# Kernel tuning notes

Hardware: AMD Instinct MI355X
Metric: run time of the kernel (lower is better)

The kernel has to match this reference:

```python
import jax, jax.numpy as jnp
import numpy as np

DIM = 256
NUM_HEADS = 4
HEAD_DIM = DIM // NUM_HEADS
SCALE = HEAD_DIM ** -0.5


def setup_inputs() -> dict:
    key = jax.random.key(0)
    ks = jax.random.split(key, 11)
    B, Nq, Nkv = 4, 2048, 2048
    inp = {
        "query_feat": jax.random.normal(ks[0], (B, Nq, DIM), dtype=jnp.float32),
        "key_value_feat": jax.random.normal(ks[1], (B, Nkv, DIM), dtype=jnp.float32),
        "reliability_kv": jax.random.uniform(ks[2], (B, Nkv), dtype=jnp.float32),
        "Wq": jax.random.normal(ks[3], (DIM, DIM), dtype=jnp.float32) * (DIM ** -0.5),
        "bq": jnp.zeros((DIM,), jnp.float32),
        "Wk": jax.random.normal(ks[4], (DIM, DIM), dtype=jnp.float32) * (DIM ** -0.5),
        "bk": jnp.zeros((DIM,), jnp.float32),
        "Wv": jax.random.normal(ks[5], (DIM, DIM), dtype=jnp.float32) * (DIM ** -0.5),
        "bv": jnp.zeros((DIM,), jnp.float32),
        "Wo": jax.random.normal(ks[6], (DIM, DIM), dtype=jnp.float32) * (DIM ** -0.5),
        "bo": jnp.zeros((DIM,), jnp.float32),
    }
    return inp


def _heads(x):
    B, N, C = x.shape
    return x.reshape(B, N, NUM_HEADS, HEAD_DIM).transpose(0, 2, 1, 3)  # [B,H,N,hd]


def reference(query_feat, key_value_feat, reliability_kv, Wq, bq, Wk, bk, Wv, bv, Wo, bo):
    B, Nq, _ = query_feat.shape
    q = _heads(query_feat @ Wq + bq)          # [B,H,Nq,hd]
    k = _heads(key_value_feat @ Wk + bk)      # [B,H,Nkv,hd]
    v = _heads(key_value_feat @ Wv + bv)
    # gate K/V by reliability (broadcast over heads and head_dim)
    rk = reliability_kv[:, None, :, None]     # [B,1,Nkv,1]
    k = k * rk
    v = v * rk
    attn = jnp.einsum("bhqd,bhkd->bhqk", q, k) * SCALE
    log_r = jnp.log(jnp.clip(reliability_kv, 1e-6))[:, None, None, :]  # [B,1,1,Nkv]
    attn = jax.nn.softmax(attn + log_r, axis=-1)  # [B,H,Nq,Nkv]
    out = jnp.einsum("bhqk,bhkd->bhqd", attn, v)
    out = out.transpose(0, 2, 1, 3).reshape(B, Nq, DIM)
    out = out @ Wo + bo
    attn_mean = attn.mean(axis=1)  # [B,Nq,Nkv]
    return out, attn_mean
```

## Files before the change

kernel.cpp:

```cpp
#include <hip/hip_runtime.h>


typedef __attribute__((ext_vector_type(8))) _Float16 half8;
typedef __attribute__((ext_vector_type(4))) _Float16 half4;
typedef __attribute__((ext_vector_type(2))) __fp16 fp16x2;
typedef __attribute__((ext_vector_type(4))) float f32x4;

#define MFMAH32(A, B, C) __builtin_amdgcn_mfma_f32_16x16x32_f16((A), (B), (C), 0, 0, 0)
#define MFMAH16(A, B, C) __builtin_amdgcn_mfma_f32_16x16x16f16((A), (B), (C), 0, 0, 0)

__device__ __forceinline__ unsigned short f2h(float f) {
    union { _Float16 h; unsigned short u; } c; c.h = (_Float16)f; return c.u;
}
__device__ __forceinline__ float h2f(unsigned short u) {
    union { unsigned short u; _Float16 h; } c; c.u = u; return (float)c.h;
}
__device__ __forceinline__ half8 ldh8(const unsigned short* p) {
    return *reinterpret_cast<const half8*>(p);
}
__device__ __forceinline__ half4 ldh4(const unsigned short* p) {
    return *reinterpret_cast<const half4*>(p);
}
__device__ __forceinline__ half4 pk4(float a, float b, float c, float d) {
    union { fp16x2 h2[2]; half4 h4; } u;
    u.h2[0] = __builtin_amdgcn_cvt_pkrtz(a, b);
    u.h2[1] = __builtin_amdgcn_cvt_pkrtz(c, d);
    return u.h4;
}
__device__ __forceinline__ void gld16(const unsigned short* g, unsigned short* l) {
    __builtin_amdgcn_global_load_lds(
        (const __attribute__((address_space(1))) unsigned int*)g,
        (__attribute__((address_space(3))) unsigned int*)l, 16, 0, 0);
}

__global__ void wsplit_kernel(const float* __restrict__ Wq, const float* __restrict__ Wk,
                              const float* __restrict__ Wv, const float* __restrict__ Wo,
                              unsigned short* __restrict__ WT) {
    int e = blockIdx.x * 256 + threadIdx.x;
    int m = e >> 16;
    int idx = e & 65535;
    int k = idx >> 8, n = idx & 255;
    const float* W = (m == 0) ? Wq : (m == 1) ? Wk : (m == 2) ? Wv : Wo;
    WT[m * 65536 + n * 256 + k] = f2h(W[idx]);
}

#define STAGE_W(dst_, src_, kt_) do {                                               \
    _Pragma("unroll")                                                               \
    for (int j_ = 0; j_ < 4; ++j_) {                                                \
        int s_ = w * 4 + j_;                                                        \
        int rowl_ = 8 * s_ + (l >> 3);                                              \
        int so_ = rowl_ * 256 + (kt_) * 64 + (((l & 7) ^ (rowl_ & 7)) << 3);        \
        gld16(&(src_)[so_], &(dst_)[s_ * 512]);                                     \
    }                                                                               \
} while (0)

#define GEMM_TILE(buf_, kt_) do {                                                   \
    _Pragma("unroll")                                                               \
    for (int ksl_ = 0; ksl_ < 2; ++ksl_) {                                          \
        _Pragma("unroll")                                                           \
        for (int n_ = 0; n_ < 16; ++n_) {                                           \
            int r_ = n_ * 16 + l15;                                                 \
            int idx_ = r_ * 64 + ((((ksl_)*4 + lg) ^ (r_ & 7)) << 3);               \
            half8 b_ = ldh8(&(buf_)[idx_]);                                         \
            acc[n_] = MFMAH32(ah[(kt_) * 2 + ksl_], b_, acc[n_]);                   \
        }                                                                           \
    }                                                                               \
} while (0)

__global__ __launch_bounds__(512, 1) void proj3_kernel(
    const float* __restrict__ query, const float* __restrict__ kv,
    const float* __restrict__ rel, const unsigned short* __restrict__ WT,
    const float* __restrict__ bq, const float* __restrict__ bk, const float* __restrict__ bv,
    unsigned short* __restrict__ Qh, unsigned short* __restrict__ Kh,
    unsigned short* __restrict__ Vtmp) {
    const int job = blockIdx.y;
    const float* X = (job == 0) ? query : kv;
    const unsigned short* wg = WT + job * 65536;
    const float* bias = (job == 0) ? bq : (job == 1) ? bk : bv;
    const float* rs = (job == 0) ? nullptr : rel;
    unsigned short* oh = (job == 0) ? Qh : (job == 1) ? Kh : Vtmp;

    __shared__ __align__(16) unsigned short wlds[2][256 * 64];

    const int w = threadIdx.x >> 6, l = threadIdx.x & 63;
    const int l15 = l & 15, lg = l >> 4;
    const int arow = blockIdx.x * 128 + w * 16 + l15;

    half8 ah[8];
#pragma unroll
    for (int ks = 0; ks < 8; ++ks) {
        const float* p = &X[arow * 256 + ks * 32 + lg * 8];
        float4 f0 = *reinterpret_cast<const float4*>(p);
        float4 f1 = *reinterpret_cast<const float4*>(p + 4);
        half8 t;
        t[0] = (_Float16)f0.x; t[1] = (_Float16)f0.y; t[2] = (_Float16)f0.z; t[3] = (_Float16)f0.w;
        t[4] = (_Float16)f1.x; t[5] = (_Float16)f1.y; t[6] = (_Float16)f1.z; t[7] = (_Float16)f1.w;
        ah[ks] = t;
    }
    f32x4 acc[16];
#pragma unroll
    for (int n = 0; n < 16; ++n) acc[n] = (f32x4){0.f, 0.f, 0.f, 0.f};

    STAGE_W(wlds[0], wg, 0);
    __syncthreads();
#pragma unroll
    for (int kt = 0; kt < 4; ++kt) {
        const int cur = kt & 1, nx = cur ^ 1;
        if (kt < 3) STAGE_W(wlds[nx], wg, kt + 1);
        GEMM_TILE(wlds[cur], kt);
        __syncthreads();
    }

    const int orow0 = blockIdx.x * 128 + w * 16 + lg * 4;
    float rsv[4];
#pragma unroll
    for (int r = 0; r < 4; ++r) rsv[r] = rs ? rs[orow0 + r] : 1.0f;
#pragma unroll
    for (int n = 0; n < 16; ++n) {
        const int col = n * 16 + l15;
        const float bn = bias[col];
#pragma unroll
        for (int r = 0; r < 4; ++r)
            oh[(orow0 + r) * 256 + col] = f2h((acc[n][r] + bn) * rsv[r]);
    }
}

__global__ void transpose_v_kernel(const unsigned short* __restrict__ Vtmp,
                                   unsigned short* __restrict__ Vt) {
    __shared__ unsigned short tile[16][264];
    const int st = blockIdx.x, b = blockIdx.y;
    const int t = threadIdx.x;
#pragma unroll
    for (int it = 0; it < 4; ++it) {
        int idx = it * 256 + t;
        int kr = idx >> 6;
        int d4 = (idx & 63) * 4;
        ushort4 v = *reinterpret_cast<const ushort4*>(
            &Vtmp[(size_t)(b * 2048 + st * 16 + kr) * 256 + d4]);
        tile[kr][d4 + 0] = v.x; tile[kr][d4 + 1] = v.y;
        tile[kr][d4 + 2] = v.z; tile[kr][d4 + 3] = v.w;
    }
    __syncthreads();
    {
        const int d = t;
        unsigned int u[8];
#pragma unroll
        for (int k2 = 0; k2 < 8; ++k2)
            u[k2] = (unsigned int)tile[k2 * 2][d] | ((unsigned int)tile[k2 * 2 + 1][d] << 16);
        uint4* dst = reinterpret_cast<uint4*>(&Vt[((size_t)(b * 128 + st) * 256 + d) * 16]);
        dst[0] = (uint4){u[0], u[1], u[2], u[3]};
        dst[1] = (uint4){u[4], u[5], u[6], u[7]};
    }
}

__global__ __launch_bounds__(512, 4) void attn_pass1(
    const unsigned short* __restrict__ Qh, const unsigned short* __restrict__ Kh,
    const unsigned short* __restrict__ Vt, const float* __restrict__ rel,
    float* __restrict__ po_a, float* __restrict__ po_b, float* __restrict__ ps) {
    const int bid = blockIdx.x;
    const int sw = (bid & 7) * 64 + (bid >> 3);
    const int b = sw >> 7;
    const int rem = sw & 127;
    const int kh = rem & 1;
    const int q0 = (rem >> 1) * 32;
    const int tid = threadIdx.x;
    const int w = tid >> 6, h = w & 3, ks = w >> 2;
    const int l = tid & 63, l15 = l & 15, lg = l >> 4;
    const float C2 = 0.18033688011112042f;

    __shared__ __align__(16) unsigned short ldsK[8][2][1024];
    __shared__ __align__(16) unsigned short ldsV[8][2][1024];
    __shared__ float rel_lr[2048];
    __shared__ float ssum_sh[2][4][2][16];

    {
        float4 v = reinterpret_cast<const float4*>(&rel[b * 2048])[tid];
        float* d = &rel_lr[tid * 4];
        d[0] = log2f(fmaxf(v.x, 1e-6f)); d[1] = log2f(fmaxf(v.y, 1e-6f));
        d[2] = log2f(fmaxf(v.z, 1e-6f)); d[3] = log2f(fmaxf(v.w, 1e-6f));
    }

    half8 qf00, qf01, qf10, qf11;
    {
        const int o0 = (b * 2048 + q0 + l15) * 256 + h * 64 + lg * 8;
        const int o1 = o0 + 16 * 256;
        qf00 = ldh8(&Qh[o0]); qf01 = ldh8(&Qh[o0 + 32]);
        qf10 = ldh8(&Qh[o1]); qf11 = ldh8(&Qh[o1 + 32]);
    }
    __syncthreads();

    const int st0 = kh * 64 + ks * 32;

#define STG(buf_, i_) do {                                                          \
    const unsigned short* kbp_ = Kh + (size_t)(b * 2048 + (st0 + (i_)) * 16) * 256  \
                                 + h * 64;                                          \
    _Pragma("unroll")                                                               \
    for (int j_ = 0; j_ < 2; ++j_) {                                                \
        int r_ = j_ * 8 + (l >> 3);                                                 \
        gld16(kbp_ + r_ * 256 + (((l & 7) ^ ((l >> 3) & 7)) << 3),                  \
              &ldsK[w][buf_][j_ * 512]);                                            \
    }                                                                               \
    const unsigned short* vbp_ = Vt + (size_t)((b * 128 + st0 + (i_)) * 256         \
                                 + h * 64) * 16;                                    \
    _Pragma("unroll")                                                               \
    for (int j_ = 0; j_ < 2; ++j_) {                                                \
        int d_ = j_ * 32 + (l >> 1);                                                \
        gld16(vbp_ + d_ * 16 + (((l & 1) ^ ((l >> 1) & 1)) << 3),                   \
              &ldsV[w][buf_][j_ * 512]);                                            \
    }                                                                               \
} while (0)

    float ssum0 = 0.f, ssum1 = 0.f;
    f32x4 o0acc[4], o1acc[4];
#pragma unroll
    for (int dc = 0; dc < 4; ++dc) {
        o0acc[dc] = (f32x4){0.f, 0.f, 0.f, 0.f};
        o1acc[dc] = (f32x4){0.f, 0.f, 0.f, 0.f};
    }

    STG(0, 0);
    for (int i = 0; i < 32; ++i) {
        const int cur = i & 1, nx = cur ^ 1;
        if (i < 31) {
            STG(nx, i + 1);
            asm volatile("s_waitcnt vmcnt(4)" ::: "memory");
        } else {
            asm volatile("s_waitcnt vmcnt(0)" ::: "memory");
        }
        __builtin_amdgcn_sched_barrier(0);
        half8 kf0 = ldh8(&ldsK[w][cur][l15 * 64 + ((lg ^ (l15 & 7)) << 3)]);
        half8 kf1 = ldh8(&ldsK[w][cur][l15 * 64 + (((4 + lg) ^ (l15 & 7)) << 3)]);
        f32x4 a0 = (f32x4){0.f, 0.f, 0.f, 0.f}, a1 = a0;
        a0 = MFMAH32(kf0, qf00, a0); a0 = MFMAH32(kf1, qf01, a0);
        a1 = MFMAH32(kf0, qf10, a1); a1 = MFMAH32(kf1, qf11, a1);
        float4 lr4 = *reinterpret_cast<const float4*>(&rel_lr[(st0 + i) * 16 + lg * 4]);
        float p00 = exp2f(__builtin_fmaf(a0[0], C2, lr4.x));
        float p01 = exp2f(__builtin_fmaf(a0[1], C2, lr4.y));
        float p02 = exp2f(__builtin_fmaf(a0[2], C2, lr4.z));
        float p03 = exp2f(__builtin_fmaf(a0[3], C2, lr4.w));
        float p10 = exp2f(__builtin_fmaf(a1[0], C2, lr4.x));
        float p11 = exp2f(__builtin_fmaf(a1[1], C2, lr4.y));
        float p12 = exp2f(__builtin_fmaf(a1[2], C2, lr4.z));
        float p13 = exp2f(__builtin_fmaf(a1[3], C2, lr4.w));
        ssum0 += (p00 + p01) + (p02 + p03);
        ssum1 += (p10 + p11) + (p12 + p13);
        half4 pa0 = pk4(p00, p01, p02, p03);
        half4 pa1 = pk4(p10, p11, p12, p13);
#pragma unroll
        for (int dc = 0; dc < 4; ++dc) {
            const int d = dc * 16 + l15;
            half4 vf = ldh4(&ldsV[w][cur][d * 16 + ((((lg >> 1) ^ (d & 1))) << 3) + (lg & 1) * 4]);
            o0acc[dc] = MFMAH16(pa0, vf, o0acc[dc]);
            o1acc[dc] = MFMAH16(pa1, vf, o1acc[dc]);
        }
    }
#undef STG

    float v0 = ssum0, v1 = ssum1;
    v0 += __shfl_xor(v0, 16); v0 += __shfl_xor(v0, 32);
    v1 += __shfl_xor(v1, 16); v1 += __shfl_xor(v1, 32);

    __syncthreads();
    if (l < 16) { ssum_sh[ks][h][0][l] = v0; ssum_sh[ks][h][1][l] = v1; }
    float* obuf = (float*)&ldsK[0][0][0];
    if (ks == 1) {
#pragma unroll
        for (int dc = 0; dc < 4; ++dc)
#pragma unroll
            for (int r = 0; r < 4; ++r) {
                const int d = h * 64 + dc * 16 + l15;
                obuf[(lg * 4 + r) * 256 + d] = o0acc[dc][r];
                obuf[(16 + lg * 4 + r) * 256 + d] = o1acc[dc][r];
            }
    }
    __syncthreads();
    if (ks == 0) {
        const int chunk = b * 2 + kh;
        float* po = (chunk < 2) ? (po_a + (size_t)chunk * 524288)
                                : (po_b + (size_t)(chunk - 2) * 524288);
#pragma unroll
        for (int dc = 0; dc < 4; ++dc)
#pragma unroll
            for (int r = 0; r < 4; ++r) {
                const int d = h * 64 + dc * 16 + l15;
                const int qa = lg * 4 + r, qb = 16 + lg * 4 + r;
                po[(size_t)(q0 + qa) * 256 + d] = o0acc[dc][r] + obuf[qa * 256 + d];
                po[(size_t)(q0 + qb) * 256 + d] = o1acc[dc][r] + obuf[qb * 256 + d];
            }
        if (l < 16) {
            ps[(chunk * 4 + h) * 2048 + q0 + l] =
                ssum_sh[0][h][0][l] + ssum_sh[1][h][0][l];
            ps[(chunk * 4 + h) * 2048 + q0 + 16 + l] =
                ssum_sh[0][h][1][l] + ssum_sh[1][h][1][l];
        }
    }
}

__global__ __launch_bounds__(256) void combine_kernel(
    const float* __restrict__ po_a, const float* __restrict__ po_b,
    const float* __restrict__ ps, unsigned short* __restrict__ AO,
    float* __restrict__ sinv_ws) {
    const int t = blockIdx.x * 256 + threadIdx.x;
    const int d4 = t & 63;
    const int bq = t >> 6;
    const int q = bq & 2047;
    const int b = bq >> 11;
    const int d0 = d4 * 4, h = d0 >> 6;
    const int c0 = b * 2, c1 = b * 2 + 1;
    const float* p0 = (c0 < 2) ? po_a + (size_t)c0 * 524288 : po_b + (size_t)(c0 - 2) * 524288;
    const float* p1 = (c1 < 2) ? po_a + (size_t)c1 * 524288 : po_b + (size_t)(c1 - 2) * 524288;
    float4 x = *reinterpret_cast<const float4*>(&p0[(size_t)q * 256 + d0]);
    float4 y = *reinterpret_cast<const float4*>(&p1[(size_t)q * 256 + d0]);
    float s = ps[(c0 * 4 + h) * 2048 + q] + ps[(c1 * 4 + h) * 2048 + q];
    float si = 1.0f / s;
    ushort4 o;
    o.x = f2h((x.x + y.x) * si); o.y = f2h((x.y + y.y) * si);
    o.z = f2h((x.z + y.z) * si); o.w = f2h((x.w + y.w) * si);
    *reinterpret_cast<ushort4*>(&AO[((size_t)(b * 2048 + q)) * 256 + d0]) = o;
    if (d4 == (h << 4)) sinv_ws[(b * 4 + h) * 2048 + q] = si;
}

__global__ __launch_bounds__(256, 4) void attn_mean_kernel(
    const unsigned short* __restrict__ Qh, const unsigned short* __restrict__ Kh,
    const float* __restrict__ rel, const float* __restrict__ sinv_ws,
    float* __restrict__ attn_mean) {
    const int kslice = blockIdx.x >> 8;
    const int inner = blockIdx.x & 255;
    const int sw = (inner & 7) * 32 + (inner >> 3);
    const int b = sw >> 6;
    const int q0 = (sw & 63) * 32;
    const int tid = threadIdx.x;
    const int w = tid >> 6;
    const int qs = w >> 1, kc = w & 1;
    const int l = tid & 63, l15 = l & 15, lg = l >> 4;
    const int kb = b * 2048;
    const float C2 = 0.18033688011112042f;

    __shared__ __align__(16) unsigned short ldsK[2][8192];
    __shared__ float rel_lr[2048];

#define STAGE_KM(dst_, kt_) do {                                                    \
    _Pragma("unroll")                                                               \
    for (int j_ = 0; j_ < 4; ++j_) {                                                \
        int s_ = w * 4 + j_;                                                        \
        int r_ = 2 * s_ + (l >> 5);                                                 \
        size_t so_ = (size_t)(kb + (kt_) * 32 + r_) * 256 +                         \
                     (((l & 31) ^ (r_ & 7)) << 3);                                  \
        gld16(&Kh[so_], &(dst_)[s_ * 512]);                                         \
    }                                                                               \
} while (0)

    {
        float4 v0 = reinterpret_cast<const float4*>(&rel[b * 2048])[tid * 2];
        float4 v1 = reinterpret_cast<const float4*>(&rel[b * 2048])[tid * 2 + 1];
        float* d = &rel_lr[tid * 8];
        d[0] = log2f(fmaxf(v0.x, 1e-6f)); d[1] = log2f(fmaxf(v0.y, 1e-6f));
        d[2] = log2f(fmaxf(v0.z, 1e-6f)); d[3] = log2f(fmaxf(v0.w, 1e-6f));
        d[4] = log2f(fmaxf(v1.x, 1e-6f)); d[5] = log2f(fmaxf(v1.y, 1e-6f));
        d[6] = log2f(fmaxf(v1.z, 1e-6f)); d[7] = log2f(fmaxf(v1.w, 1e-6f));
    }

    half8 qf[4][2];
    {
        const int qrow = b * 2048 + q0 + qs * 16 + l15;
#pragma unroll
        for (int h = 0; h < 4; ++h)
#pragma unroll
            for (int kd = 0; kd < 2; ++kd)
                qf[h][kd] = ldh8(&Qh[qrow * 256 + h * 64 + kd * 32 + lg * 8]);
    }
    float lsi[4][4];
#pragma unroll
    for (int h = 0; h < 4; ++h)
#pragma unroll
        for (int r4 = 0; r4 < 4; ++r4)
            lsi[h][r4] = log2f(sinv_ws[(b * 4 + h) * 2048 + q0 + qs * 16 + lg * 4 + r4]) - 2.0f;
    __syncthreads();

    const int kt0 = kslice * 8;
    STAGE_KM(ldsK[0], kt0);
    for (int ki = 0; ki < 8; ++ki) {
        const int kt = kt0 + ki;
        const int cur = ki & 1, nx = cur ^ 1;
        if (ki < 7) {
            STAGE_KM(ldsK[nx], kt + 1);
            asm volatile("s_waitcnt vmcnt(4)" ::: "memory");
        } else {
            asm volatile("s_waitcnt vmcnt(0)" ::: "memory");
        }
        asm volatile("s_barrier" ::: "memory");
        __builtin_amdgcn_sched_barrier(0);
        const int r = kc * 16 + l15;
        const int rx = r & 7;
        f32x4 a[4];
#pragma unroll
        for (int h = 0; h < 4; ++h) {
            half8 kf0 = ldh8(&ldsK[cur][r * 256 + (((h * 8 + lg) ^ rx) << 3)]);
            half8 kf1 = ldh8(&ldsK[cur][r * 256 + (((h * 8 + 4 + lg) ^ rx) << 3)]);
            f32x4 t = (f32x4){0.f, 0.f, 0.f, 0.f};
            t = MFMAH32(qf[h][0], kf0, t);
            t = MFMAH32(qf[h][1], kf1, t);
            a[h] = t;
        }
        const float lr = rel_lr[kt * 32 + kc * 16 + l15];
        const size_t kcol = (size_t)(kt * 32 + kc * 16 + l15);
#pragma unroll
        for (int r4 = 0; r4 < 4; ++r4) {
            float m = exp2f(__builtin_fmaf(a[0][r4], C2, lsi[0][r4]) + lr)
                    + exp2f(__builtin_fmaf(a[1][r4], C2, lsi[1][r4]) + lr)
                    + exp2f(__builtin_fmaf(a[2][r4], C2, lsi[2][r4]) + lr)
                    + exp2f(__builtin_fmaf(a[3][r4], C2, lsi[3][r4]) + lr);
            attn_mean[(size_t)(b * 2048 + q0 + qs * 16 + lg * 4 + r4) * 2048 + kcol] = m;
        }
        asm volatile("s_waitcnt lgkmcnt(0)\n\ts_barrier" ::: "memory");
    }
#undef STAGE_KM
}

__global__ __launch_bounds__(512, 1) void final_kernel(
    const unsigned short* __restrict__ AO, const unsigned short* __restrict__ WoT,
    const float* __restrict__ bo, float* __restrict__ out) {
    __shared__ __align__(16) unsigned short wlds[2][256 * 64];

    const int w = threadIdx.x >> 6, l = threadIdx.x & 63;
    const int l15 = l & 15, lg = l >> 4;
    const int arow = blockIdx.x * 128 + w * 16 + l15;

    half8 ah[8];
#pragma unroll
    for (int ks = 0; ks < 8; ++ks)
        ah[ks] = ldh8(&AO[arow * 256 + ks * 32 + lg * 8]);
    f32x4 acc[16];
#pragma unroll
    for (int n = 0; n < 16; ++n) acc[n] = (f32x4){0.f, 0.f, 0.f, 0.f};

    STAGE_W(wlds[0], WoT, 0);
    __syncthreads();
#pragma unroll
    for (int kt = 0; kt < 4; ++kt) {
        const int cur = kt & 1, nx = cur ^ 1;
        if (kt < 3) STAGE_W(wlds[nx], WoT, kt + 1);
        GEMM_TILE(wlds[cur], kt);
        __syncthreads();
    }

    const int orow0 = blockIdx.x * 128 + w * 16 + lg * 4;
#pragma unroll
    for (int n = 0; n < 16; ++n) {
        const int col = n * 16 + l15;
        const float bn = bo[col];
#pragma unroll
        for (int r = 0; r < 4; ++r)
            out[(orow0 + r) * 256 + col] = acc[n][r] + bn;
    }
}

extern "C" void kernel_launch(void* const* d_in, const int* in_sizes, int n_in,
                              void* d_out, int out_size, void* d_ws, size_t ws_size,
                              hipStream_t stream) {
    const float* query = (const float*)d_in[0];
    const float* kv    = (const float*)d_in[1];
    const float* rel   = (const float*)d_in[2];
    const float* Wq    = (const float*)d_in[3];
    const float* bq    = (const float*)d_in[4];
    const float* Wk    = (const float*)d_in[5];
    const float* bk    = (const float*)d_in[6];
    const float* Wv    = (const float*)d_in[7];
    const float* bv    = (const float*)d_in[8];
    const float* Wo    = (const float*)d_in[9];
    const float* bo    = (const float*)d_in[10];

    char* ws = (char*)d_ws;
    unsigned short* WT   = (unsigned short*)(ws + 0);
    unsigned short* Qh   = (unsigned short*)(ws + 524288);
    unsigned short* Kh   = (unsigned short*)(ws + 4718592);
    unsigned short* Vtmp = (unsigned short*)(ws + 8912896);
    unsigned short* Vt   = (unsigned short*)(ws + 13107200);
    unsigned short* AO   = (unsigned short*)(ws + 17301504);
    float*          sinv = (float*)(ws + 21495808);
    float*          ps   = (float*)(ws + 21626880);
    float*          po_b = (float*)(ws + 21889024);
    float*          po_a = (float*)Vtmp;

    float* out = (float*)d_out;
    float* attn_mean = (float*)d_out + 2097152;

    wsplit_kernel<<<1024, 256, 0, stream>>>(Wq, Wk, Wv, Wo, WT);
    proj3_kernel<<<dim3(64, 3), 512, 0, stream>>>(query, kv, rel, WT,
                                                  bq, bk, bv, Qh, Kh, Vtmp);
    transpose_v_kernel<<<dim3(128, 4), 256, 0, stream>>>(Vtmp, Vt);
    attn_pass1<<<512, 512, 0, stream>>>(Qh, Kh, Vt, rel, po_a, po_b, ps);
    combine_kernel<<<2048, 256, 0, stream>>>(po_a, po_b, ps, AO, sinv);
    attn_mean_kernel<<<2048, 256, 0, stream>>>(Qh, Kh, rel, sinv, attn_mean);
    final_kernel<<<64, 512, 0, stream>>>(AO, WT + 3 * 65536, bo, out);
}
```

Measured before the change: 111.8 us.

## Double query tile per block in attention pass and attn_mean kernels

In attn_pass1 each block now handles 64 query rows instead of 32, reusing every staged K/V tile across four 16-row query fragments, and the grid is halved. In attn_mean_kernel each wave now covers both 16-key column chunks for its own 16-row slice of a 64-row query tile, so every Q fragment is reused over more keys and the grid is halved. This cuts K/V global and LDS traffic per unit of work, at the cost of more accumulator registers (launch bounds lowered to 2 blocks per SM) and fewer blocks to spread across the GPU's compute units.

After: 109.8 us. Within noise of the previous version (-1.8%).

```diff
diff --git a/kernel.cpp b/kernel.cpp
--- a/kernel.cpp
+++ b/kernel.cpp
@@ -153,25 +153,24 @@
     }
 }
 
-__global__ __launch_bounds__(512, 4) void attn_pass1(
+__global__ __launch_bounds__(512, 2) void attn_pass1(
     const unsigned short* __restrict__ Qh, const unsigned short* __restrict__ Kh,
     const unsigned short* __restrict__ Vt, const float* __restrict__ rel,
     float* __restrict__ po_a, float* __restrict__ po_b, float* __restrict__ ps) {
     const int bid = blockIdx.x;
-    const int sw = (bid & 7) * 64 + (bid >> 3);
-    const int b = sw >> 7;
-    const int rem = sw & 127;
+    const int sw = (bid & 7) * 32 + (bid >> 3);
+    const int b = sw >> 6;
+    const int rem = sw & 63;
     const int kh = rem & 1;
-    const int q0 = (rem >> 1) * 32;
+    const int q0 = (rem >> 1) * 64;
     const int tid = threadIdx.x;
     const int w = tid >> 6, h = w & 3, ks = w >> 2;
     const int l = tid & 63, l15 = l & 15, lg = l >> 4;
     const float C2 = 0.18033688011112042f;
 
-    __shared__ __align__(16) unsigned short ldsK[8][2][1024];
-    __shared__ __align__(16) unsigned short ldsV[8][2][1024];
+    __shared__ __align__(16) unsigned short ldsKV[2][8][2][1024];
     __shared__ float rel_lr[2048];
-    __shared__ float ssum_sh[2][4][2][16];
+    __shared__ float ssum_sh[2][4][64];
 
     {
         float4 v = reinterpret_cast<const float4*>(&rel[b * 2048])[tid];
@@ -180,13 +179,13 @@
         d[2] = log2f(fmaxf(v.z, 1e-6f)); d[3] = log2f(fmaxf(v.w, 1e-6f));
     }
 
-    half8 qf00, qf01, qf10, qf11;
-    {
-        const int o0 = (b * 2048 + q0 + l15) * 256 + h * 64 + lg * 8;
-        const int o1 = o0 + 16 * 256;
-        qf00 = ldh8(&Qh[o0]); qf01 = ldh8(&Qh[o0 + 32]);
-        qf10 = ldh8(&Qh[o1]); qf11 = ldh8(&Qh[o1 + 32]);
-    }
+    half8 qf[4][2];
+#pragma unroll
+    for (int qs = 0; qs < 4; ++qs)
+#pragma unroll
+        for (int kd = 0; kd < 2; ++kd)
+            qf[qs][kd] = ldh8(&Qh[(b * 2048 + q0 + qs * 16 + l15) * 256 +
+                                  h * 64 + kd * 32 + lg * 8]);
     __syncthreads();
 
     const int st0 = kh * 64 + ks * 32;
@@ -198,7 +197,7 @@
     for (int j_ = 0; j_ < 2; ++j_) {                                                \
         int r_ = j_ * 8 + (l >> 3);                                                 \
         gld16(kbp_ + r_ * 256 + (((l & 7) ^ ((l >> 3) & 7)) << 3),                  \
-              &ldsK[w][buf_][j_ * 512]);                                            \
+              &ldsKV[0][w][buf_][j_ * 512]);                                        \
     }                                                                               \
     const unsigned short* vbp_ = Vt + (size_t)((b * 128 + st0 + (i_)) * 256         \
                                  + h * 64) * 16;                                    \
@@ -206,17 +205,17 @@
     for (int j_ = 0; j_ < 2; ++j_) {                                                \
         int d_ = j_ * 32 + (l >> 1);                                                \
         gld16(vbp_ + d_ * 16 + (((l & 1) ^ ((l >> 1) & 1)) << 3),                   \
-              &ldsV[w][buf_][j_ * 512]);                                            \
+              &ldsKV[1][w][buf_][j_ * 512]);                                        \
     }                                                                               \
 } while (0)
 
-    float ssum0 = 0.f, ssum1 = 0.f;
-    f32x4 o0acc[4], o1acc[4];
-#pragma unroll
-    for (int dc = 0; dc < 4; ++dc) {
-        o0acc[dc] = (f32x4){0.f, 0.f, 0.f, 0.f};
-        o1acc[dc] = (f32x4){0.f, 0.f, 0.f, 0.f};
-    }
+    float ssum[4] = {0.f, 0.f, 0.f, 0.f};
+    f32x4 oacc[4][4];
+#pragma unroll
+    for (int qs = 0; qs < 4; ++qs)
+#pragma unroll
+        for (int dc = 0; dc < 4; ++dc)
+            oacc[qs][dc] = (f32x4){0.f, 0.f, 0.f, 0.f};
 
     STG(0, 0);
     for (int i = 0; i < 32; ++i) {
@@ -228,50 +227,63 @@
             asm volatile("s_waitcnt vmcnt(0)" ::: "memory");
         }
         __builtin_amdgcn_sched_barrier(0);
-        half8 kf0 = ldh8(&ldsK[w][cur][l15 * 64 + ((lg ^ (l15 & 7)) << 3)]);
-        half8 kf1 = ldh8(&ldsK[w][cur][l15 * 64 + (((4 + lg) ^ (l15 & 7)) << 3)]);
-        f32x4 a0 = (f32x4){0.f, 0.f, 0.f, 0.f}, a1 = a0;
-        a0 = MFMAH32(kf0, qf00, a0); a0 = MFMAH32(kf1, qf01, a0);
-        a1 = MFMAH32(kf0, qf10, a1); a1 = MFMAH32(kf1, qf11, a1);
+        half8 kf0 = ldh8(&ldsKV[0][w][cur][l15 * 64 + ((lg ^ (l15 & 7)) << 3)]);
+        half8 kf1 = ldh8(&ldsKV[0][w][cur][l15 * 64 + (((4 + lg) ^ (l15 & 7)) << 3)]);
+        f32x4 a[4];
+#pragma unroll
+        for (int qs = 0; qs < 4; ++qs) {
+            f32x4 t = (f32x4){0.f, 0.f, 0.f, 0.f};
+            t = MFMAH32(kf0, qf[qs][0], t);
+            t = MFMAH32(kf1, qf[qs][1], t);
+            a[qs] = t;
+        }
         float4 lr4 = *reinterpret_cast<const float4*>(&rel_lr[(st0 + i) * 16 + lg * 4]);
-        float p00 = exp2f(__builtin_fmaf(a0[0], C2, lr4.x));
-        float p01 = exp2f(__builtin_fmaf(a0[1], C2, lr4.y));
-        float p02 = exp2f(__builtin_fmaf(a0[2], C2, lr4.z));
-        float p03 = exp2f(__builtin_fmaf(a0[3], C2, lr4.w));
-        float p10 = exp2f(__builtin_fmaf(a1[0], C2, lr4.x));
-        float p11 = exp2f(__builtin_fmaf(a1[1], C2, lr4.y));
-        float p12 = exp2f(__builtin_fmaf(a1[2], C2, lr4.z));
-        float p13 = exp2f(__builtin_fmaf(a1[3], C2, lr4.w));
-        ssum0 += (p00 + p01) + (p02 + p03);
-        ssum1 += (p10 + p11) + (p12 + p13);
-        half4 pa0 = pk4(p00, p01, p02, p03);
-        half4 pa1 = pk4(p10, p11, p12, p13);
+        half4 pa[4];
+#pragma unroll
+        for (int qs = 0; qs < 4; ++qs) {
+            float p0 = exp2f(__builtin_fmaf(a[qs][0], C2, lr4.x));
+            float p1 = exp2f(__builtin_fmaf(a[qs][1], C2, lr4.y));
+            float p2 = exp2f(__builtin_fmaf(a[qs][2], C2, lr4.z));
+            float p3 = exp2f(__builtin_fmaf(a[qs][3], C2, lr4.w));
+            ssum[qs] += (p0 + p1) + (p2 + p3);
+            pa[qs] = pk4(p0, p1, p2, p3);
+        }
 #pragma unroll
         for (int dc = 0; dc < 4; ++dc) {
             const int d = dc * 16 + l15;
-            half4 vf = ldh4(&ldsV[w][cur][d * 16 + ((((lg >> 1) ^ (d & 1))) << 3) + (lg & 1) * 4]);
-            o0acc[dc] = MFMAH16(pa0, vf, o0acc[dc]);
-            o1acc[dc] = MFMAH16(pa1, vf, o1acc[dc]);
+            half4 vf = ldh4(&ldsKV[1][w][cur][d * 16 +
+                            ((((lg >> 1) ^ (d & 1))) << 3) + (lg & 1) * 4]);
+#pragma unroll
+            for (int qs = 0; qs < 4; ++qs)
+                oacc[qs][dc] = MFMAH16(pa[qs], vf, oacc[qs][dc]);
         }
     }
 #undef STG
 
-    float v0 = ssum0, v1 = ssum1;
-    v0 += __shfl_xor(v0, 16); v0 += __shfl_xor(v0, 32);
-    v1 += __shfl_xor(v1, 16); v1 += __shfl_xor(v1, 32);
-
-    __syncthreads();
-    if (l < 16) { ssum_sh[ks][h][0][l] = v0; ssum_sh[ks][h][1][l] = v1; }
-    float* obuf = (float*)&ldsK[0][0][0];
+    float vred[4];
+#pragma unroll
+    for (int qs = 0; qs < 4; ++qs) {
+        float v = ssum[qs];
+        v += __shfl_xor(v, 16); v += __shfl_xor(v, 32);
+        vred[qs] = v;
+    }
+
+    __syncthreads();
+    if (l < 16) {
+#pragma unroll
+        for (int qs = 0; qs < 4; ++qs)
+            ssum_sh[ks][h][qs * 16 + l] = vred[qs];
+    }
+    float* obuf = (float*)&ldsKV[0][0][0][0];
     if (ks == 1) {
 #pragma unroll
-        for (int dc = 0; dc < 4; ++dc)
-#pragma unroll
-            for (int r = 0; r < 4; ++r) {
-                const int d = h * 64 + dc * 16 + l15;
-                obuf[(lg * 4 + r) * 256 + d] = o0acc[dc][r];
-                obuf[(16 + lg * 4 + r) * 256 + d] = o1acc[dc][r];
-            }
+        for (int qs = 0; qs < 4; ++qs)
+#pragma unroll
+            for (int dc = 0; dc < 4; ++dc)
+#pragma unroll
+                for (int r = 0; r < 4; ++r)
+                    obuf[(qs * 16 + lg * 4 + r) * 256 + h * 64 + dc * 16 + l15] =
+                        oacc[qs][dc][r];
     }
     __syncthreads();
     if (ks == 0) {
@@ -279,19 +291,20 @@
         float* po = (chunk < 2) ? (po_a + (size_t)chunk * 524288)
                                 : (po_b + (size_t)(chunk - 2) * 524288);
 #pragma unroll
-        for (int dc = 0; dc < 4; ++dc)
-#pragma unroll
-            for (int r = 0; r < 4; ++r) {
-                const int d = h * 64 + dc * 16 + l15;
-                const int qa = lg * 4 + r, qb = 16 + lg * 4 + r;
-                po[(size_t)(q0 + qa) * 256 + d] = o0acc[dc][r] + obuf[qa * 256 + d];
-                po[(size_t)(q0 + qb) * 256 + d] = o1acc[dc][r] + obuf[qb * 256 + d];
-            }
+        for (int qs = 0; qs < 4; ++qs)
+#pragma unroll
+            for (int dc = 0; dc < 4; ++dc)
+#pragma unroll
+                for (int r = 0; r < 4; ++r) {
+                    const int d = h * 64 + dc * 16 + l15;
+                    const int q = qs * 16 + lg * 4 + r;
+                    po[(size_t)(q0 + q) * 256 + d] = oacc[qs][dc][r] + obuf[q * 256 + d];
+                }
         if (l < 16) {
-            ps[(chunk * 4 + h) * 2048 + q0 + l] =
-                ssum_sh[0][h][0][l] + ssum_sh[1][h][0][l];
-            ps[(chunk * 4 + h) * 2048 + q0 + 16 + l] =
-                ssum_sh[0][h][1][l] + ssum_sh[1][h][1][l];
+#pragma unroll
+            for (int qs = 0; qs < 4; ++qs)
+                ps[(chunk * 4 + h) * 2048 + q0 + qs * 16 + l] =
+                    ssum_sh[0][h][qs * 16 + l] + ssum_sh[1][h][qs * 16 + l];
         }
     }
 }
@@ -324,14 +337,13 @@
     const unsigned short* __restrict__ Qh, const unsigned short* __restrict__ Kh,
     const float* __restrict__ rel, const float* __restrict__ sinv_ws,
     float* __restrict__ attn_mean) {
-    const int kslice = blockIdx.x >> 8;
-    const int inner = blockIdx.x & 255;
-    const int sw = (inner & 7) * 32 + (inner >> 3);
-    const int b = sw >> 6;
-    const int q0 = (sw & 63) * 32;
+    const int kslice = blockIdx.x >> 7;
+    const int inner = blockIdx.x & 127;
+    const int sw = (inner & 7) * 16 + (inner >> 3);
+    const int b = sw >> 5;
+    const int q0 = (sw & 31) * 64;
     const int tid = threadIdx.x;
     const int w = tid >> 6;
-    const int qs = w >> 1, kc = w & 1;
     const int l = tid & 63, l15 = l & 15, lg = l >> 4;
     const int kb = b * 2048;
     const float C2 = 0.18033688011112042f;
@@ -362,7 +374,7 @@
 
     half8 qf[4][2];
     {
-        const int qrow = b * 2048 + q0 + qs * 16 + l15;
+        const int qrow = b * 2048 + q0 + w * 16 + l15;
 #pragma unroll
         for (int h = 0; h < 4; ++h)
 #pragma unroll
@@ -374,7 +386,7 @@
     for (int h = 0; h < 4; ++h)
 #pragma unroll
         for (int r4 = 0; r4 < 4; ++r4)
-            lsi[h][r4] = log2f(sinv_ws[(b * 4 + h) * 2048 + q0 + qs * 16 + lg * 4 + r4]) - 2.0f;
+            lsi[h][r4] = log2f(sinv_ws[(b * 4 + h) * 2048 + q0 + w * 16 + lg * 4 + r4]) - 2.0f;
     __syncthreads();
 
     const int kt0 = kslice * 8;
@@ -390,27 +402,30 @@
         }
         asm volatile("s_barrier" ::: "memory");
         __builtin_amdgcn_sched_barrier(0);
-        const int r = kc * 16 + l15;
-        const int rx = r & 7;
-        f32x4 a[4];
-#pragma unroll
-        for (int h = 0; h < 4; ++h) {
-            half8 kf0 = ldh8(&ldsK[cur][r * 256 + (((h * 8 + lg) ^ rx) << 3)]);
-            half8 kf1 = ldh8(&ldsK[cur][r * 256 + (((h * 8 + 4 + lg) ^ rx) << 3)]);
-            f32x4 t = (f32x4){0.f, 0.f, 0.f, 0.f};
-            t = MFMAH32(qf[h][0], kf0, t);
-            t = MFMAH32(qf[h][1], kf1, t);
-            a[h] = t;
-        }
-        const float lr = rel_lr[kt * 32 + kc * 16 + l15];
-        const size_t kcol = (size_t)(kt * 32 + kc * 16 + l15);
-#pragma unroll
-        for (int r4 = 0; r4 < 4; ++r4) {
-            float m = exp2f(__builtin_fmaf(a[0][r4], C2, lsi[0][r4]) + lr)
-                    + exp2f(__builtin_fmaf(a[1][r4], C2, lsi[1][r4]) + lr)
-                    + exp2f(__builtin_fmaf(a[2][r4], C2, lsi[2][r4]) + lr)
-                    + exp2f(__builtin_fmaf(a[3][r4], C2, lsi[3][r4]) + lr);
-            attn_mean[(size_t)(b * 2048 + q0 + qs * 16 + lg * 4 + r4) * 2048 + kcol] = m;
+#pragma unroll
+        for (int kc = 0; kc < 2; ++kc) {
+            const int r = kc * 16 + l15;
+            const int rx = r & 7;
+            f32x4 a[4];
+#pragma unroll
+            for (int h = 0; h < 4; ++h) {
+                half8 kf0 = ldh8(&ldsK[cur][r * 256 + (((h * 8 + lg) ^ rx) << 3)]);
+                half8 kf1 = ldh8(&ldsK[cur][r * 256 + (((h * 8 + 4 + lg) ^ rx) << 3)]);
+                f32x4 t = (f32x4){0.f, 0.f, 0.f, 0.f};
+                t = MFMAH32(qf[h][0], kf0, t);
+                t = MFMAH32(qf[h][1], kf1, t);
+                a[h] = t;
+            }
+            const float lr = rel_lr[kt * 32 + kc * 16 + l15];
+            const size_t kcol = (size_t)(kt * 32 + kc * 16 + l15);
+#pragma unroll
+            for (int r4 = 0; r4 < 4; ++r4) {
+                float m = exp2f(__builtin_fmaf(a[0][r4], C2, lsi[0][r4]) + lr)
+                        + exp2f(__builtin_fmaf(a[1][r4], C2, lsi[1][r4]) + lr)
+                        + exp2f(__builtin_fmaf(a[2][r4], C2, lsi[2][r4]) + lr)
+                        + exp2f(__builtin_fmaf(a[3][r4], C2, lsi[3][r4]) + lr);
+                attn_mean[(size_t)(b * 2048 + q0 + w * 16 + lg * 4 + r4) * 2048 + kcol] = m;
+            }
         }
         asm volatile("s_waitcnt lgkmcnt(0)\n\ts_barrier" ::: "memory");
     }
@@ -489,8 +504,8 @@
     proj3_kernel<<<dim3(64, 3), 512, 0, stream>>>(query, kv, rel, WT,
                                                   bq, bk, bv, Qh, Kh, Vtmp);
     transpose_v_kernel<<<dim3(128, 4), 256, 0, stream>>>(Vtmp, Vt);
-    attn_pass1<<<512, 512, 0, stream>>>(Qh, Kh, Vt, rel, po_a, po_b, ps);
+    attn_pass1<<<256, 512, 0, stream>>>(Qh, Kh, Vt, rel, po_a, po_b, ps);
     combine_kernel<<<2048, 256, 0, stream>>>(po_a, po_b, ps, AO, sinv);
-    attn_mean_kernel<<<2048, 256, 0, stream>>>(Qh, Kh, rel, sinv, attn_mean);
+    attn_mean_kernel<<<1024, 256, 0, stream>>>(Qh, Kh, rel, sinv, attn_mean);
     final_kernel<<<64, 512, 0, stream>>>(AO, WT + 3 * 65536, bo, out);
 }
```
